# Optimization experiments

Measured on AMD Instinct MI355X. Metric: run time of the kernel, lower is better.

The kernel has to match this reference:

```python
import jax, jax.numpy as jnp
import numpy as np

N_NODES = 100000
NEG_SLOPE = 0.01  # F.leaky_relu default


def setup_inputs() -> dict:
    key = jax.random.key(0)
    k1, k2, k3, k4, k5 = jax.random.split(key, 5)
    x = jax.random.normal(k1, (N_NODES, 128), dtype=jnp.float32)
    edge_index = jax.random.randint(k2, (2, 1600000), 0, N_NODES, dtype=jnp.int64)
    # GCNConv linear weights (PyG: x @ W.T), bias added after aggregation
    W1 = jax.random.normal(k3, (128, 128), dtype=jnp.float32) * (1.0 / np.sqrt(128))
    b1 = jnp.zeros((128,), dtype=jnp.float32)
    W2 = jax.random.normal(k4, (128, 128), dtype=jnp.float32) * (1.0 / np.sqrt(128))
    b2 = jnp.zeros((128,), dtype=jnp.float32)
    return {"x": x, "edge_index": edge_index, "W1": W1, "b1": b1, "W2": W2, "b2": b2}


def _gcn_layer(x, W, b, src, dst, norm, self_w):
    # linear transform first (GCNConv order): h = x @ W.T
    h = x @ W.T
    # message passing: sum_j norm_ij * h_j  (edges) + self-loop term h_i / deg_i
    msg = h[src] * norm[:, None]                       # [E, F] gather (memory-bound)
    agg = jax.ops.segment_sum(msg, dst, num_segments=x.shape[0])
    out = agg + h * self_w[:, None] + b
    return out


def reference(x, edge_index, W1, b1, W2, b2):
    src = edge_index[0]
    dst = edge_index[1]
    n = x.shape[0]
    # gcn_norm with self-loops: deg_i = in-degree(dst) + 1
    deg = jax.ops.segment_sum(jnp.ones_like(dst, dtype=x.dtype), dst, num_segments=n) + 1.0
    deg_inv_sqrt = jax.lax.rsqrt(deg)
    norm = deg_inv_sqrt[src] * deg_inv_sqrt[dst]       # edge weights
    self_w = deg_inv_sqrt * deg_inv_sqrt               # self-loop weight = 1/deg

    h = _gcn_layer(x, W1, b1, src, dst, norm, self_w)
    h = jax.nn.leaky_relu(h, NEG_SLOPE)
    # dropout inactive (eval semantics)
    h = _gcn_layer(h, W2, b2, src, dst, norm, self_w)
    h = jax.nn.leaky_relu(h, NEG_SLOPE)
    return h
```

## Files before the change

kernel.cpp:

```cpp
#include <hip/hip_runtime.h>

#define F 128
#define NEG_SLOPE 0.01f
#define NPB 256
#define PMAX 512
#define HB 4096
#define BB 8192
#define CAP 6144

typedef _Float16 half8_t __attribute__((ext_vector_type(8)));
typedef float f32x4 __attribute__((ext_vector_type(4)));


__global__ __launch_bounds__(512) void zero_bcnt(int* __restrict__ bcnt) {
    bcnt[threadIdx.x] = 0;
}

__global__ __launch_bounds__(256) void hist_kernel(const int* __restrict__ dst,
                                                   int* __restrict__ bcnt,
                                                   int E, int nP) {
    __shared__ int h[PMAX];
    int tid = threadIdx.x;
    for (int i = tid; i < nP; i += 256) h[i] = 0;
    __syncthreads();
    int base = blockIdx.x * HB;
    for (int i = tid; i < HB && base + i < E; i += 256)
        atomicAdd(&h[dst[base + i] >> 8], 1);
    __syncthreads();
    for (int i = tid; i < nP; i += 256)
        if (h[i]) atomicAdd(&bcnt[i], h[i]);
}

__global__ __launch_bounds__(512) void scan_bk(const int* __restrict__ bcnt,
                                               int* __restrict__ bbase,
                                               int* __restrict__ bcur, int nP) {
    __shared__ int s[512];
    int tid = threadIdx.x;
    int v = (tid < nP) ? bcnt[tid] : 0;
    int run = v;
    s[tid] = v;
    __syncthreads();
    for (int off = 1; off < 512; off <<= 1) {
        int add = (tid >= off) ? s[tid - off] : 0;
        __syncthreads();
        run += add;
        s[tid] = run;
        __syncthreads();
    }
    if (tid < nP) { bbase[tid] = run - v; bcur[tid] = run - v; }
}

__global__ __launch_bounds__(256) void bin_kernel(const int* __restrict__ src,
                                                  const int* __restrict__ dst,
                                                  int* __restrict__ bcur,
                                                  int* __restrict__ binned,
                                                  int E, int nP) {
    __shared__ int hist[PMAX];
    __shared__ int lbase[PMAX];
    __shared__ int gbase[PMAX];
    __shared__ int cur[PMAX];
    __shared__ int sa[PMAX];
    __shared__ int buf[BB];
    __shared__ unsigned short b16[BB];
    int tid = threadIdx.x;
    int base = blockIdx.x * BB;
    int myE = E - base; if (myE > BB) myE = BB;

    for (int i = tid; i < nP; i += 256) hist[i] = 0;
    __syncthreads();
    for (int i = tid; i < myE; i += 256)
        atomicAdd(&hist[dst[base + i] >> 8], 1);
    __syncthreads();
    {
        int j0 = tid, j1 = tid + 256;
        sa[j0] = (j0 < nP) ? hist[j0] : 0;
        sa[j1] = (j1 < nP) ? hist[j1] : 0;
        __syncthreads();
        for (int off = 1; off < PMAX; off <<= 1) {
            int t0 = sa[j0] + (j0 >= off ? sa[j0 - off] : 0);
            int t1 = sa[j1] + (j1 >= off ? sa[j1 - off] : 0);
            __syncthreads();
            sa[j0] = t0; sa[j1] = t1;
            __syncthreads();
        }
        if (j0 < nP) { lbase[j0] = sa[j0] - hist[j0]; cur[j0] = sa[j0] - hist[j0]; }
        if (j1 < nP) { lbase[j1] = sa[j1] - hist[j1]; cur[j1] = sa[j1] - hist[j1]; }
    }
    __syncthreads();
    for (int i = tid; i < nP; i += 256)
        gbase[i] = hist[i] ? atomicAdd(&bcur[i], hist[i]) : 0;
    __syncthreads();
    for (int i = tid; i < myE; i += 256) {
        int d = dst[base + i], s = src[base + i];
        int b = d >> 8;
        int lp = atomicAdd(&cur[b], 1);
        buf[lp] = ((d & (NPB - 1)) << 17) | s;
        b16[lp] = (unsigned short)b;
    }
    __syncthreads();
    for (int j = tid; j < myE; j += 256) {
        int b = b16[j];
        binned[gbase[b] + (j - lbase[b])] = buf[j];
    }
}

__global__ __launch_bounds__(256) void csr_kernel(const int* __restrict__ binned,
                                                  const int* __restrict__ bcnt,
                                                  const int* __restrict__ bbase,
                                                  int* __restrict__ srcs,
                                                  int* __restrict__ offs,
                                                  float* __restrict__ dis, int N) {
    __shared__ int cnt[NPB];
    __shared__ int tmp[NPB];
    __shared__ int cur[NPB];
    __shared__ int buf[CAP];
    int tid = threadIdx.x;
    int b = blockIdx.x;
    int ebase = bbase[b];
    int count = bcnt[b];
    int lo = b << 8;
    cnt[tid] = 0;
    __syncthreads();
    for (int j = tid; j < count; j += 256)
        atomicAdd(&cnt[binned[ebase + j] >> 17], 1);
    __syncthreads();
    int v = cnt[tid];
    int run = v;
    tmp[tid] = v;
    __syncthreads();
    for (int off = 1; off < 256; off <<= 1) {
        int add = (tid >= off) ? tmp[tid - off] : 0;
        __syncthreads();
        run += add;
        tmp[tid] = run;
        __syncthreads();
    }
    int excl = run - v;
    cur[tid] = excl;
    int node = lo + tid;
    if (node < N) {
        offs[node] = ebase + excl;
        dis[node] = rsqrtf((float)v + 1.0f);
    }
    __syncthreads();
    for (int j = tid; j < count; j += 256) {
        int rec = binned[ebase + j];
        int pos = atomicAdd(&cur[rec >> 17], 1);
        int s = rec & 0x1FFFF;
        if (pos < CAP) buf[pos] = s; else srcs[ebase + pos] = s;
    }
    __syncthreads();
    int lim = count < CAP ? count : CAP;
    for (int j = tid; j < lim; j += 256)
        srcs[ebase + j] = buf[j];
}


__global__ __launch_bounds__(256) void cvt_w(const float* __restrict__ W1,
                                             const float* __restrict__ W2,
                                             _Float16* __restrict__ W1h,
                                             _Float16* __restrict__ W2h) {
    int i = blockIdx.x * 256 + threadIdx.x;
    const int n4 = F * F / 4;
    const float* in = (i < n4) ? W1 : W2;
    _Float16* out = (i < n4) ? W1h : W2h;
    int j = (i < n4) ? i : i - n4;
    float4 v = ((const float4*)in)[j];
    half8_t h;
    h[0] = (_Float16)v.x; h[1] = (_Float16)v.y;
    h[2] = (_Float16)v.z; h[3] = (_Float16)v.w;
    *(int2*)&((_Float16*)out)[j * 4] = *(int2*)&h;
}


__device__ __forceinline__ void gemm_core(const half8_t afrag[4],
                                          const _Float16* __restrict__ Wh,
                                          const float* __restrict__ dis,
                                          int tile, int m, int quad,
                                          _Float16* __restrict__ orow) {
    f32x4 acc[8];
#pragma unroll
    for (int t = 0; t < 8; ++t) acc[t] = (f32x4){0.f, 0.f, 0.f, 0.f};
#pragma unroll
    for (int c = 0; c < 4; ++c) {
#pragma unroll
        for (int t = 0; t < 8; ++t) {
            half8_t bfrag = *(const half8_t*)&Wh[(t * 16 + m) * F + c * 32 + quad * 8];
            acc[t] = __builtin_amdgcn_mfma_f32_16x16x32_f16(afrag[c], bfrag, acc[t],
                                                            0, 0, 0);
        }
    }
    float d[4];
#pragma unroll
    for (int r = 0; r < 4; ++r) d[r] = dis[tile * 16 + quad * 4 + r];
#pragma unroll
    for (int t = 0; t < 8; ++t)
#pragma unroll
        for (int r = 0; r < 4; ++r)
            orow[(quad * 4 + r) * F + t * 16 + m] = (_Float16)(acc[t][r] * d[r]);
}

__global__ __launch_bounds__(256) void gemm_a32(const float* __restrict__ A,
                                                const _Float16* __restrict__ Wh,
                                                const float* __restrict__ dis,
                                                _Float16* __restrict__ out,
                                                int ntiles) {
    int wave = threadIdx.x >> 6;
    int lane = threadIdx.x & 63;
    int tile = blockIdx.x * 4 + wave;
    if (tile >= ntiles) return;
    int m = lane & 15, quad = lane >> 4;
    const float* arow = A + (size_t)tile * 16 * F;
    half8_t afrag[4];
#pragma unroll
    for (int c = 0; c < 4; ++c) {
        float4 t0 = *(const float4*)&arow[m * F + c * 32 + quad * 8];
        float4 t1 = *(const float4*)&arow[m * F + c * 32 + quad * 8 + 4];
        afrag[c][0] = (_Float16)t0.x; afrag[c][1] = (_Float16)t0.y;
        afrag[c][2] = (_Float16)t0.z; afrag[c][3] = (_Float16)t0.w;
        afrag[c][4] = (_Float16)t1.x; afrag[c][5] = (_Float16)t1.y;
        afrag[c][6] = (_Float16)t1.z; afrag[c][7] = (_Float16)t1.w;
    }
    gemm_core(afrag, Wh, dis, tile, m, quad, out + (size_t)tile * 16 * F);
}

__global__ __launch_bounds__(256) void gemm_a16(const _Float16* __restrict__ A,
                                                const _Float16* __restrict__ Wh,
                                                const float* __restrict__ dis,
                                                _Float16* __restrict__ out,
                                                int ntiles) {
    int wave = threadIdx.x >> 6;
    int lane = threadIdx.x & 63;
    int tile = blockIdx.x * 4 + wave;
    if (tile >= ntiles) return;
    int m = lane & 15, quad = lane >> 4;
    const _Float16* arow = A + (size_t)tile * 16 * F;
    half8_t afrag[4];
#pragma unroll
    for (int c = 0; c < 4; ++c)
        afrag[c] = *(const half8_t*)&arow[m * F + c * 32 + quad * 8];
    gemm_core(afrag, Wh, dis, tile, m, quad, out + (size_t)tile * 16 * F);
}


#define AGG_BODY(H8)                                                           \
    int node = blockIdx.x * 4 + (threadIdx.x >> 6);                            \
    int lane = threadIdx.x & 63;                                               \
    if (node >= n) return;                                                     \
    int g = lane >> 4;                                                         \
    int fo = lane & 15;                                                        \
    int beg = offs[node];                                                      \
    int end = (node + 1 < n) ? offs[node + 1] : E;                             \
    float acc[8];                                                              \
    _Pragma("unroll") for (int j = 0; j < 8; ++j) acc[j] = 0.f;                \
    if (beg < end) {                                                           \
        int i0 = beg + g, i1 = beg + 4 + g;                                    \
        int s0 = srcs[i0 < end ? i0 : beg];                                    \
        int s1 = srcs[i1 < end ? i1 : beg];                                    \
        float w0 = (i0 < end) ? 1.f : 0.f;                                     \
        float w1 = (i1 < end) ? 1.f : 0.f;                                     \
        for (int e = beg; e < end; e += 8) {                                   \
            int ns0 = s0, ns1 = s1;                                            \
            float nw0 = 0.f, nw1 = 0.f;                                        \
            if (e + 8 < end) {                                                 \
                int j0 = e + 8 + g, j1 = e + 12 + g;                           \
                ns0 = srcs[j0 < end ? j0 : beg];                               \
                ns1 = srcs[j1 < end ? j1 : beg];                               \
                nw0 = (j0 < end) ? 1.f : 0.f;                                  \
                nw1 = (j1 < end) ? 1.f : 0.f;                                  \
            }                                                                  \
            half8_t a0 = H8[(size_t)s0 * 16 + fo];                             \
            half8_t a1 = H8[(size_t)s1 * 16 + fo];                             \
            _Pragma("unroll") for (int j = 0; j < 8; ++j)                      \
                acc[j] += w0 * (float)a0[j] + w1 * (float)a1[j];               \
            s0 = ns0; s1 = ns1; w0 = nw0; w1 = nw1;                            \
        }                                                                      \
    }                                                                          \
    _Pragma("unroll") for (int j = 0; j < 8; ++j) {                            \
        acc[j] += __shfl_xor(acc[j], 16);                                      \
        acc[j] += __shfl_xor(acc[j], 32);                                      \
    }                                                                          \
    if (lane >= 16) return;                                                    \
    float di = dis[node];                                                      \
    half8_t hv = H8[(size_t)node * 16 + fo];                                   \
    float4 b0 = ((const float4*)bias)[fo * 2];                                 \
    float4 b1v = ((const float4*)bias)[fo * 2 + 1];                            \
    acc[0] = di * (acc[0] + (float)hv[0]) + b0.x;                              \
    acc[1] = di * (acc[1] + (float)hv[1]) + b0.y;                              \
    acc[2] = di * (acc[2] + (float)hv[2]) + b0.z;                              \
    acc[3] = di * (acc[3] + (float)hv[3]) + b0.w;                              \
    acc[4] = di * (acc[4] + (float)hv[4]) + b1v.x;                             \
    acc[5] = di * (acc[5] + (float)hv[5]) + b1v.y;                             \
    acc[6] = di * (acc[6] + (float)hv[6]) + b1v.z;                             \
    acc[7] = di * (acc[7] + (float)hv[7]) + b1v.w;                             \
    _Pragma("unroll") for (int j = 0; j < 8; ++j)                              \
        acc[j] = (acc[j] > 0.f) ? acc[j] : acc[j] * NEG_SLOPE;

__global__ __launch_bounds__(256) void agg_to_h(const half8_t* __restrict__ h8,
                                                const float* __restrict__ dis,
                                                const float* __restrict__ bias,
                                                const int* __restrict__ srcs,
                                                const int* __restrict__ offs,
                                                half8_t* __restrict__ out,
                                                int n, int E) {
    AGG_BODY(h8)
    half8_t o;
#pragma unroll
    for (int j = 0; j < 8; ++j) o[j] = (_Float16)acc[j];
    out[(size_t)node * 16 + fo] = o;
}

__global__ __launch_bounds__(256) void agg_to_f(const half8_t* __restrict__ h8,
                                                const float* __restrict__ dis,
                                                const float* __restrict__ bias,
                                                const int* __restrict__ srcs,
                                                const int* __restrict__ offs,
                                                float* __restrict__ out,
                                                int n, int E) {
    AGG_BODY(h8)
    float4 o0 = make_float4(acc[0], acc[1], acc[2], acc[3]);
    float4 o1 = make_float4(acc[4], acc[5], acc[6], acc[7]);
    ((float4*)out)[(size_t)node * 32 + fo * 2] = o0;
    ((float4*)out)[(size_t)node * 32 + fo * 2 + 1] = o1;
}


static inline size_t alup(size_t x) { return (x + 255) & ~(size_t)255; }

extern "C" void kernel_launch(void* const* d_in, const int* in_sizes, int n_in,
                              void* d_out, int out_size, void* d_ws, size_t ws_size,
                              hipStream_t stream) {
    const float* x  = (const float*)d_in[0];
    const int*   ei = (const int*)d_in[1];
    const float* W1 = (const float*)d_in[2];
    const float* b1 = (const float*)d_in[3];
    const float* W2 = (const float*)d_in[4];
    const float* b2 = (const float*)d_in[5];
    float* out = (float*)d_out;

    const int N = in_sizes[0] / F;
    const int E = in_sizes[1] / 2;
    const int* src = ei;
    const int* dst = ei + E;

    char* p = (char*)d_ws;
    int*      bcnt   = (int*)p;      p += alup(PMAX * 4);
    int*      bbase  = (int*)p;      p += alup(PMAX * 4);
    int*      bcur   = (int*)p;      p += alup(PMAX * 4);
    float*    dis    = (float*)p;    p += alup((size_t)N * 4);
    int*      offs   = (int*)p;      p += alup((size_t)N * 4);
    int*      binned = (int*)p;      p += alup((size_t)E * 4);
    int*      srcs   = (int*)p;      p += alup((size_t)E * 4);
    _Float16* g      = (_Float16*)p; p += alup((size_t)N * F * 2);
    _Float16* hh     = (_Float16*)p; p += alup((size_t)N * F * 2);
    _Float16* W1h    = (_Float16*)p; p += alup((size_t)F * F * 2);
    _Float16* W2h    = (_Float16*)p; p += alup((size_t)F * F * 2);

    const int nP = (N + NPB - 1) / NPB;
    const int ntiles = (N + 15) / 16;
    const int gemm_grid = (ntiles + 3) / 4;

    zero_bcnt<<<1, 512, 0, stream>>>(bcnt);
    hist_kernel<<<(E + HB - 1) / HB, 256, 0, stream>>>(dst, bcnt, E, nP);
    scan_bk<<<1, 512, 0, stream>>>(bcnt, bbase, bcur, nP);
    bin_kernel<<<(E + BB - 1) / BB, 256, 0, stream>>>(src, dst, bcur, binned, E, nP);
    csr_kernel<<<nP, 256, 0, stream>>>(binned, bcnt, bbase, srcs, offs, dis, N);
    cvt_w<<<(2 * F * F / 4 + 255) / 256, 256, 0, stream>>>(W1, W2, W1h, W2h);

    gemm_a32<<<gemm_grid, 256, 0, stream>>>(x, W1h, dis, hh, ntiles);
    agg_to_h<<<(N + 3) / 4, 256, 0, stream>>>((const half8_t*)hh, dis, b1, srcs,
                                              offs, (half8_t*)g, N, E);
    gemm_a16<<<gemm_grid, 256, 0, stream>>>(g, W2h, dis, hh, ntiles);
    agg_to_f<<<(N + 3) / 4, 256, 0, stream>>>((const half8_t*)hh, dis, b2, srcs,
                                              offs, out, N, E);
}
```

Baseline: 342.0 us.

## Fold weight conversion into histogram kernel and widen aggregation gather loop

The separate weight fp32-to-fp16 conversion kernel is removed and its work is done by 32 extra blocks appended to the histogram kernel, which saves one launch. The aggregation loop drops its software-pipelined prefetch of source indices and instead issues four neighbor-row gathers per iteration (16 edges per wave per step) rather than two. The per-node self term, degree scale and bias loads are hoisted ahead of the loop so they overlap with the gathers. More loads in flight per step should hide gather latency better, at the cost of more wasted lanes when a node has few neighbors and more registers per thread.

```diff
diff --git a/kernel.cpp b/kernel.cpp
--- a/kernel.cpp
+++ b/kernel.cpp
@@ -18,9 +18,27 @@
 
 __global__ __launch_bounds__(256) void hist_kernel(const int* __restrict__ dst,
                                                    int* __restrict__ bcnt,
-                                                   int E, int nP) {
+                                                   int E, int nP,
+                                                   const float* __restrict__ W1,
+                                                   const float* __restrict__ W2,
+                                                   _Float16* __restrict__ W1h,
+                                                   _Float16* __restrict__ W2h) {
     __shared__ int h[PMAX];
     int tid = threadIdx.x;
+    int hb = gridDim.x - 32;
+    if (blockIdx.x >= hb) {
+        int i = (blockIdx.x - hb) * 256 + tid;
+        const int n4 = F * F / 4;
+        const float* in = (i < n4) ? W1 : W2;
+        _Float16* out = (i < n4) ? W1h : W2h;
+        int j = (i < n4) ? i : i - n4;
+        float4 v = ((const float4*)in)[j];
+        half8_t hx;
+        hx[0] = (_Float16)v.x; hx[1] = (_Float16)v.y;
+        hx[2] = (_Float16)v.z; hx[3] = (_Float16)v.w;
+        *(int2*)&((_Float16*)out)[j * 4] = *(int2*)&hx;
+        return;
+    }
     for (int i = tid; i < nP; i += 256) h[i] = 0;
     __syncthreads();
     int base = blockIdx.x * HB;
@@ -156,23 +174,6 @@
 }
 
 
-__global__ __launch_bounds__(256) void cvt_w(const float* __restrict__ W1,
-                                             const float* __restrict__ W2,
-                                             _Float16* __restrict__ W1h,
-                                             _Float16* __restrict__ W2h) {
-    int i = blockIdx.x * 256 + threadIdx.x;
-    const int n4 = F * F / 4;
-    const float* in = (i < n4) ? W1 : W2;
-    _Float16* out = (i < n4) ? W1h : W2h;
-    int j = (i < n4) ? i : i - n4;
-    float4 v = ((const float4*)in)[j];
-    half8_t h;
-    h[0] = (_Float16)v.x; h[1] = (_Float16)v.y;
-    h[2] = (_Float16)v.z; h[3] = (_Float16)v.w;
-    *(int2*)&((_Float16*)out)[j * 4] = *(int2*)&h;
-}
-
-
 __device__ __forceinline__ void gemm_core(const half8_t afrag[4],
                                           const _Float16* __restrict__ Wh,
                                           const float* __restrict__ dis,
@@ -243,7 +244,7 @@
 }
 
 
-#define AGG_BODY(H8)                                                           \
+#define AGG_BODY(H8, STORE)                                                    \
     int node = blockIdx.x * 4 + (threadIdx.x >> 6);                            \
     int lane = threadIdx.x & 63;                                               \
     if (node >= n) return;                                                     \
@@ -251,40 +252,35 @@
     int fo = lane & 15;                                                        \
     int beg = offs[node];                                                      \
     int end = (node + 1 < n) ? offs[node + 1] : E;                             \
+    float di = dis[node];                                                      \
+    half8_t hv = H8[(size_t)node * 16 + fo];                                   \
+    float4 b0 = ((const float4*)bias)[fo * 2];                                 \
+    float4 b1v = ((const float4*)bias)[fo * 2 + 1];                            \
     float acc[8];                                                              \
     _Pragma("unroll") for (int j = 0; j < 8; ++j) acc[j] = 0.f;                \
-    if (beg < end) {                                                           \
-        int i0 = beg + g, i1 = beg + 4 + g;                                    \
+    for (int e = beg; e < end; e += 16) {                                      \
+        int i0 = e + g, i1 = e + 4 + g, i2 = e + 8 + g, i3 = e + 12 + g;       \
         int s0 = srcs[i0 < end ? i0 : beg];                                    \
         int s1 = srcs[i1 < end ? i1 : beg];                                    \
+        int s2 = srcs[i2 < end ? i2 : beg];                                    \
+        int s3 = srcs[i3 < end ? i3 : beg];                                    \
         float w0 = (i0 < end) ? 1.f : 0.f;                                     \
         float w1 = (i1 < end) ? 1.f : 0.f;                                     \
-        for (int e = beg; e < end; e += 8) {                                   \
-            int ns0 = s0, ns1 = s1;                                            \
-            float nw0 = 0.f, nw1 = 0.f;                                        \
-            if (e + 8 < end) {                                                 \
-                int j0 = e + 8 + g, j1 = e + 12 + g;                           \
-                ns0 = srcs[j0 < end ? j0 : beg];                               \
-                ns1 = srcs[j1 < end ? j1 : beg];                               \
-                nw0 = (j0 < end) ? 1.f : 0.f;                                  \
-                nw1 = (j1 < end) ? 1.f : 0.f;                                  \
-            }                                                                  \
-            half8_t a0 = H8[(size_t)s0 * 16 + fo];                             \
-            half8_t a1 = H8[(size_t)s1 * 16 + fo];                             \
-            _Pragma("unroll") for (int j = 0; j < 8; ++j)                      \
-                acc[j] += w0 * (float)a0[j] + w1 * (float)a1[j];               \
-            s0 = ns0; s1 = ns1; w0 = nw0; w1 = nw1;                            \
-        }                                                                      \
+        float w2 = (i2 < end) ? 1.f : 0.f;                                     \
+        float w3 = (i3 < end) ? 1.f : 0.f;                                     \
+        half8_t a0 = H8[(size_t)s0 * 16 + fo];                                 \
+        half8_t a1 = H8[(size_t)s1 * 16 + fo];                                 \
+        half8_t a2 = H8[(size_t)s2 * 16 + fo];                                 \
+        half8_t a3 = H8[(size_t)s3 * 16 + fo];                                 \
+        _Pragma("unroll") for (int j = 0; j < 8; ++j)                          \
+            acc[j] += (w0 * (float)a0[j] + w1 * (float)a1[j]) +                \
+                      (w2 * (float)a2[j] + w3 * (float)a3[j]);                 \
     }                                                                          \
     _Pragma("unroll") for (int j = 0; j < 8; ++j) {                            \
         acc[j] += __shfl_xor(acc[j], 16);                                      \
         acc[j] += __shfl_xor(acc[j], 32);                                      \
     }                                                                          \
     if (lane >= 16) return;                                                    \
-    float di = dis[node];                                                      \
-    half8_t hv = H8[(size_t)node * 16 + fo];                                   \
-    float4 b0 = ((const float4*)bias)[fo * 2];                                 \
-    float4 b1v = ((const float4*)bias)[fo * 2 + 1];                            \
     acc[0] = di * (acc[0] + (float)hv[0]) + b0.x;                              \
     acc[1] = di * (acc[1] + (float)hv[1]) + b0.y;                              \
     acc[2] = di * (acc[2] + (float)hv[2]) + b0.z;                              \
@@ -303,7 +299,7 @@
                                                 const int* __restrict__ offs,
                                                 half8_t* __restrict__ out,
                                                 int n, int E) {
-    AGG_BODY(h8)
+    AGG_BODY(h8, )
     half8_t o;
 #pragma unroll
     for (int j = 0; j < 8; ++j) o[j] = (_Float16)acc[j];
@@ -317,7 +313,7 @@
                                                 const int* __restrict__ offs,
                                                 float* __restrict__ out,
                                                 int n, int E) {
-    AGG_BODY(h8)
+    AGG_BODY(h8, )
     float4 o0 = make_float4(acc[0], acc[1], acc[2], acc[3]);
     float4 o1 = make_float4(acc[4], acc[5], acc[6], acc[7]);
     ((float4*)out)[(size_t)node * 32 + fo * 2] = o0;
@@ -359,18 +355,19 @@
     const int nP = (N + NPB - 1) / NPB;
     const int ntiles = (N + 15) / 16;
     const int gemm_grid = (ntiles + 3) / 4;
+    const int agg_grid = (N + 3) / 4;
 
     zero_bcnt<<<1, 512, 0, stream>>>(bcnt);
-    hist_kernel<<<(E + HB - 1) / HB, 256, 0, stream>>>(dst, bcnt, E, nP);
+    hist_kernel<<<(E + HB - 1) / HB + 32, 256, 0, stream>>>(dst, bcnt, E, nP,
+                                                            W1, W2, W1h, W2h);
     scan_bk<<<1, 512, 0, stream>>>(bcnt, bbase, bcur, nP);
     bin_kernel<<<(E + BB - 1) / BB, 256, 0, stream>>>(src, dst, bcur, binned, E, nP);
     csr_kernel<<<nP, 256, 0, stream>>>(binned, bcnt, bbase, srcs, offs, dis, N);
-    cvt_w<<<(2 * F * F / 4 + 255) / 256, 256, 0, stream>>>(W1, W2, W1h, W2h);
 
     gemm_a32<<<gemm_grid, 256, 0, stream>>>(x, W1h, dis, hh, ntiles);
-    agg_to_h<<<(N + 3) / 4, 256, 0, stream>>>((const half8_t*)hh, dis, b1, srcs,
-                                              offs, (half8_t*)g, N, E);
+    agg_to_h<<<agg_grid, 256, 0, stream>>>((const half8_t*)hh, dis, b1, srcs,
+                                           offs, (half8_t*)g, N, E);
     gemm_a16<<<gemm_grid, 256, 0, stream>>>(g, W2h, dis, hh, ntiles);
-    agg_to_f<<<(N + 3) / 4, 256, 0, stream>>>((const half8_t*)hh, dis, b2, srcs,
-                                              offs, out, N, E);
-}
+    agg_to_f<<<agg_grid, 256, 0, stream>>>((const half8_t*)hh, dis, b2, srcs,
+                                           offs, out, N, E);
+}
```

New measurement: 342.5 us. No clear change (+0.2%).

## Widen CSR buckets to 512 nodes and fold scan and weight conversion into neighbors

Applied to the files above, without the earlier changes.

Doubles nodes per bucket (NPB 512, PMAX 256) so the bucket scan fits one 256-thread pass. The separate scan kernel is removed: each bin_kernel block redundantly scans the global bucket counts, and block 0 writes bbase. Weight fp16 conversion moves into extra blocks of hist_kernel, which cuts launches from 10 to 8. The aggregation kernels now issue their per-node loads (dis, self features, bias) before the edge loop, and csr_kernel's larger per-bucket counts raise its shared-memory use and per-block serial work.

```diff
diff --git a/kernel.cpp b/kernel.cpp
--- a/kernel.cpp
+++ b/kernel.cpp
@@ -2,57 +2,60 @@
 
 #define F 128
 #define NEG_SLOPE 0.01f
-#define NPB 256
-#define PMAX 512
-#define HB 4096
+#define NPB 512
+#define PMAX 256
+#define HB 8192
 #define BB 8192
-#define CAP 6144
+#define CAP 12288
 
 typedef _Float16 half8_t __attribute__((ext_vector_type(8)));
 typedef float f32x4 __attribute__((ext_vector_type(4)));
 
 
-__global__ __launch_bounds__(512) void zero_bcnt(int* __restrict__ bcnt) {
-    bcnt[threadIdx.x] = 0;
+__global__ __launch_bounds__(512) void zero_bcnt(int* __restrict__ bcnt,
+                                                 int* __restrict__ bcur) {
+    int tid = threadIdx.x;
+    if (tid < PMAX) bcnt[tid] = 0;
+    else bcur[tid - PMAX] = 0;
 }
 
 __global__ __launch_bounds__(256) void hist_kernel(const int* __restrict__ dst,
                                                    int* __restrict__ bcnt,
-                                                   int E, int nP) {
+                                                   int E, int nP,
+                                                   const float* __restrict__ W1,
+                                                   const float* __restrict__ W2,
+                                                   _Float16* __restrict__ W1h,
+                                                   _Float16* __restrict__ W2h) {
     __shared__ int h[PMAX];
     int tid = threadIdx.x;
-    for (int i = tid; i < nP; i += 256) h[i] = 0;
+    int hb = gridDim.x - 32;
+    if (blockIdx.x >= hb) {
+        int i = (blockIdx.x - hb) * 256 + tid;
+        const int n4 = F * F / 4;
+        const float* in = (i < n4) ? W1 : W2;
+        _Float16* out = (i < n4) ? W1h : W2h;
+        int j = (i < n4) ? i : i - n4;
+        float4 v = ((const float4*)in)[j];
+        half8_t hx;
+        hx[0] = (_Float16)v.x; hx[1] = (_Float16)v.y;
+        hx[2] = (_Float16)v.z; hx[3] = (_Float16)v.w;
+        *(int2*)&((_Float16*)out)[j * 4] = *(int2*)&hx;
+        return;
+    }
+    if (tid < PMAX) h[tid] = 0;
     __syncthreads();
     int base = blockIdx.x * HB;
     for (int i = tid; i < HB && base + i < E; i += 256)
-        atomicAdd(&h[dst[base + i] >> 8], 1);
-    __syncthreads();
-    for (int i = tid; i < nP; i += 256)
-        if (h[i]) atomicAdd(&bcnt[i], h[i]);
-}
-
-__global__ __launch_bounds__(512) void scan_bk(const int* __restrict__ bcnt,
-                                               int* __restrict__ bbase,
-                                               int* __restrict__ bcur, int nP) {
-    __shared__ int s[512];
-    int tid = threadIdx.x;
-    int v = (tid < nP) ? bcnt[tid] : 0;
-    int run = v;
-    s[tid] = v;
-    __syncthreads();
-    for (int off = 1; off < 512; off <<= 1) {
-        int add = (tid >= off) ? s[tid - off] : 0;
-        __syncthreads();
-        run += add;
-        s[tid] = run;
-        __syncthreads();
-    }
-    if (tid < nP) { bbase[tid] = run - v; bcur[tid] = run - v; }
+        atomicAdd(&h[dst[base + i] >> 9], 1);
+    __syncthreads();
+    if (tid < nP && h[tid]) atomicAdd(&bcnt[tid], h[tid]);
 }
 
 __global__ __launch_bounds__(256) void bin_kernel(const int* __restrict__ src,
                                                   const int* __restrict__ dst,
+                                                  const int* __restrict__ bcnt,
                                                   int* __restrict__ bcur,
+                                                  int* __restrict__ bbase,
                                                   int* __restrict__ binned,
                                                   int E, int nP) {
     __shared__ int hist[PMAX];
@@ -60,46 +63,61 @@
     __shared__ int gbase[PMAX];
     __shared__ int cur[PMAX];
     __shared__ int sa[PMAX];
+    __shared__ int sb[PMAX];
     __shared__ int buf[BB];
-    __shared__ unsigned short b16[BB];
+    __shared__ unsigned char b8[BB];
     int tid = threadIdx.x;
     int base = blockIdx.x * BB;
     int myE = E - base; if (myE > BB) myE = BB;
 
-    for (int i = tid; i < nP; i += 256) hist[i] = 0;
+    hist[tid] = 0;
     __syncthreads();
     for (int i = tid; i < myE; i += 256)
-        atomicAdd(&hist[dst[base + i] >> 8], 1);
+        atomicAdd(&hist[dst[base + i] >> 9], 1);
     __syncthreads();
     {
-        int j0 = tid, j1 = tid + 256;
-        sa[j0] = (j0 < nP) ? hist[j0] : 0;
-        sa[j1] = (j1 < nP) ? hist[j1] : 0;
+        int v = (tid < nP) ? hist[tid] : 0;
+        int run = v;
+        sa[tid] = v;
         __syncthreads();
         for (int off = 1; off < PMAX; off <<= 1) {
-            int t0 = sa[j0] + (j0 >= off ? sa[j0 - off] : 0);
-            int t1 = sa[j1] + (j1 >= off ? sa[j1 - off] : 0);
+            int add = (tid >= off) ? sa[tid - off] : 0;
             __syncthreads();
-            sa[j0] = t0; sa[j1] = t1;
+            run += add;
+            sa[tid] = run;
             __syncthreads();
         }
-        if (j0 < nP) { lbase[j0] = sa[j0] - hist[j0]; cur[j0] = sa[j0] - hist[j0]; }
-        if (j1 < nP) { lbase[j1] = sa[j1] - hist[j1]; cur[j1] = sa[j1] - hist[j1]; }
-    }
-    __syncthreads();
-    for (int i = tid; i < nP; i += 256)
-        gbase[i] = hist[i] ? atomicAdd(&bcur[i], hist[i]) : 0;
+        if (tid < nP) { lbase[tid] = run - v; cur[tid] = run - v; }
+    }
+    {
+        int v = (tid < nP) ? bcnt[tid] : 0;
+        int run = v;
+        sb[tid] = v;
+        __syncthreads();
+        for (int off = 1; off < PMAX; off <<= 1) {
+            int add = (tid >= off) ? sb[tid - off] : 0;
+            __syncthreads();
+            run += add;
+            sb[tid] = run;
+            __syncthreads();
+        }
+        int gexc = run - v;
+        if (tid < nP) {
+            if (blockIdx.x == 0) bbase[tid] = gexc;
+            gbase[tid] = hist[tid] ? gexc + atomicAdd(&bcur[tid], hist[tid]) : 0;
+        }
+    }
     __syncthreads();
     for (int i = tid; i < myE; i += 256) {
         int d = dst[base + i], s = src[base + i];
-        int b = d >> 8;
+        int b = d >> 9;
         int lp = atomicAdd(&cur[b], 1);
         buf[lp] = ((d & (NPB - 1)) << 17) | s;
-        b16[lp] = (unsigned short)b;
+        b8[lp] = (unsigned char)b;
     }
     __syncthreads();
     for (int j = tid; j < myE; j += 256) {
-        int b = b16[j];
+        int b = b8[j];
         binned[gbase[b] + (j - lbase[b])] = buf[j];
     }
 }
@@ -118,30 +136,29 @@
     int b = blockIdx.x;
     int ebase = bbase[b];
     int count = bcnt[b];
-    int lo = b << 8;
+    int lo = b << 9;
     cnt[tid] = 0;
+    cnt[tid + 256] = 0;
     __syncthreads();
     for (int j = tid; j < count; j += 256)
         atomicAdd(&cnt[binned[ebase + j] >> 17], 1);
     __syncthreads();
-    int v = cnt[tid];
-    int run = v;
-    tmp[tid] = v;
-    __syncthreads();
-    for (int off = 1; off < 256; off <<= 1) {
-        int add = (tid >= off) ? tmp[tid - off] : 0;
+    int j0 = tid, j1 = tid + 256;
+    int v0 = cnt[j0], v1 = cnt[j1];
+    tmp[j0] = v0; tmp[j1] = v1;
+    __syncthreads();
+    for (int off = 1; off < NPB; off <<= 1) {
+        int t0 = tmp[j0] + (j0 >= off ? tmp[j0 - off] : 0);
+        int t1 = tmp[j1] + (j1 >= off ? tmp[j1 - off] : 0);
         __syncthreads();
-        run += add;
-        tmp[tid] = run;
+        tmp[j0] = t0; tmp[j1] = t1;
         __syncthreads();
     }
-    int excl = run - v;
-    cur[tid] = excl;
-    int node = lo + tid;
-    if (node < N) {
-        offs[node] = ebase + excl;
-        dis[node] = rsqrtf((float)v + 1.0f);
-    }
+    int e0 = tmp[j0] - v0, e1 = tmp[j1] - v1;
+    cur[j0] = e0; cur[j1] = e1;
+    int n0 = lo + j0, n1 = lo + j1;
+    if (n0 < N) { offs[n0] = ebase + e0; dis[n0] = rsqrtf((float)v0 + 1.0f); }
+    if (n1 < N) { offs[n1] = ebase + e1; dis[n1] = rsqrtf((float)v1 + 1.0f); }
     __syncthreads();
     for (int j = tid; j < count; j += 256) {
         int rec = binned[ebase + j];
@@ -153,23 +170,6 @@
     int lim = count < CAP ? count : CAP;
     for (int j = tid; j < lim; j += 256)
         srcs[ebase + j] = buf[j];
-}
-
-
-__global__ __launch_bounds__(256) void cvt_w(const float* __restrict__ W1,
-                                             const float* __restrict__ W2,
-                                             _Float16* __restrict__ W1h,
-                                             _Float16* __restrict__ W2h) {
-    int i = blockIdx.x * 256 + threadIdx.x;
-    const int n4 = F * F / 4;
-    const float* in = (i < n4) ? W1 : W2;
-    _Float16* out = (i < n4) ? W1h : W2h;
-    int j = (i < n4) ? i : i - n4;
-    float4 v = ((const float4*)in)[j];
-    half8_t h;
-    h[0] = (_Float16)v.x; h[1] = (_Float16)v.y;
-    h[2] = (_Float16)v.z; h[3] = (_Float16)v.w;
-    *(int2*)&((_Float16*)out)[j * 4] = *(int2*)&h;
 }
 
 
@@ -251,6 +251,10 @@
     int fo = lane & 15;                                                        \
     int beg = offs[node];                                                      \
     int end = (node + 1 < n) ? offs[node + 1] : E;                             \
+    float di = dis[node];                                                      \
+    half8_t hv = H8[(size_t)node * 16 + fo];                                   \
+    float4 b0 = ((const float4*)bias)[fo * 2];                                 \
+    float4 b1v = ((const float4*)bias)[fo * 2 + 1];                            \
     float acc[8];                                                              \
     _Pragma("unroll") for (int j = 0; j < 8; ++j) acc[j] = 0.f;                \
     if (beg < end) {                                                           \
@@ -281,10 +285,6 @@
         acc[j] += __shfl_xor(acc[j], 32);                                      \
     }                                                                          \
     if (lane >= 16) return;                                                    \
-    float di = dis[node];                                                      \
-    half8_t hv = H8[(size_t)node * 16 + fo];                                   \
-    float4 b0 = ((const float4*)bias)[fo * 2];                                 \
-    float4 b1v = ((const float4*)bias)[fo * 2 + 1];                            \
     acc[0] = di * (acc[0] + (float)hv[0]) + b0.x;                              \
     acc[1] = di * (acc[1] + (float)hv[1]) + b0.y;                              \
     acc[2] = di * (acc[2] + (float)hv[2]) + b0.z;                              \
@@ -359,18 +359,19 @@
     const int nP = (N + NPB - 1) / NPB;
     const int ntiles = (N + 15) / 16;
     const int gemm_grid = (ntiles + 3) / 4;
-
-    zero_bcnt<<<1, 512, 0, stream>>>(bcnt);
-    hist_kernel<<<(E + HB - 1) / HB, 256, 0, stream>>>(dst, bcnt, E, nP);
-    scan_bk<<<1, 512, 0, stream>>>(bcnt, bbase, bcur, nP);
-    bin_kernel<<<(E + BB - 1) / BB, 256, 0, stream>>>(src, dst, bcur, binned, E, nP);
+    const int agg_grid = (N + 3) / 4;
+
+    zero_bcnt<<<1, 512, 0, stream>>>(bcnt, bcur);
+    hist_kernel<<<(E + HB - 1) / HB + 32, 256, 0, stream>>>(dst, bcnt, E, nP,
+                                                            W1, W2, W1h, W2h);
+    bin_kernel<<<(E + BB - 1) / BB, 256, 0, stream>>>(src, dst, bcnt, bcur,
+                                                      bbase, binned, E, nP);
     csr_kernel<<<nP, 256, 0, stream>>>(binned, bcnt, bbase, srcs, offs, dis, N);
-    cvt_w<<<(2 * F * F / 4 + 255) / 256, 256, 0, stream>>>(W1, W2, W1h, W2h);
 
     gemm_a32<<<gemm_grid, 256, 0, stream>>>(x, W1h, dis, hh, ntiles);
-    agg_to_h<<<(N + 3) / 4, 256, 0, stream>>>((const half8_t*)hh, dis, b1, srcs,
-                                              offs, (half8_t*)g, N, E);
+    agg_to_h<<<agg_grid, 256, 0, stream>>>((const half8_t*)hh, dis, b1, srcs,
+                                           offs, (half8_t*)g, N, E);
     gemm_a16<<<gemm_grid, 256, 0, stream>>>(g, W2h, dis, hh, ntiles);
-    agg_to_f<<<(N + 3) / 4, 256, 0, stream>>>((const half8_t*)hh, dis, b2, srcs,
-                                              offs, out, N, E);
-}
+    agg_to_f<<<agg_grid, 256, 0, stream>>>((const half8_t*)hh, dis, b2, srcs,
+                                           offs, out, N, E);
+}
```

Measured after the change: 340.3 us. About the same (-0.5%).
